# Kernel tuning notes

Measured on AMD Instinct MI355X. Metric: run time of the kernel, lower is better.

## Reference

```python
import jax, jax.numpy as jnp
import numpy as np
from jax import lax

B, C, H, W = 8, 128, 128, 128
KW = 9                      # conv window width (w == h == 9)
PW = (KW - 1) // 2


def _make_kernel(key):
    # torch kaiming_normal_(fan_out) on weight (C,1,KW,C): fan_out = C * KW * C
    std = float(np.sqrt(2.0 / (C * KW * C)))
    # stored directly in WIO layout: [KW, C_in, C_out]
    return (jax.random.normal(key, (KW, C, C), dtype=jnp.float32) * std)


def setup_inputs() -> dict:
    key = jax.random.key(0)
    kx, k1, k2, k3, k4 = jax.random.split(key, 5)
    x = jax.random.normal(kx, (B, C, H, W), dtype=jnp.float32)
    return {
        "x": x,
        "k_td": _make_kernel(k1),
        "k_dt": _make_kernel(k2),
        "k_lr": _make_kernel(k3),
        "k_rl": _make_kernel(k4),
    }


def _row_conv(y, K):
    # y: [B, W, C] -> 1D conv along W, full channel mixing, no bias
    return lax.conv_general_dilated(
        y, K, window_strides=(1,), padding=[(PW, PW)],
        dimension_numbers=("NWC", "WIO", "NWC"))


def _dir_scan(x, K, reverse):
    # x: [B, H, W, C]; sequential recurrence along axis 1:
    #   row[i] = row[i] + relu(conv(row[i-1]))   (row[i-1] already updated)
    if reverse:
        x = x[:, ::-1]
    def step(prev, cur):
        new = cur + jax.nn.relu(_row_conv(prev, K))
        return new, new
    first = x[:, 0]
    _, rest = lax.scan(step, first, jnp.moveaxis(x[:, 1:], 1, 0))
    out = jnp.concatenate([first[:, None], jnp.moveaxis(rest, 0, 1)], axis=1)
    if reverse:
        out = out[:, ::-1]
    return out


def reference(x, k_td, k_dt, k_lr, k_rl):
    y = jnp.transpose(x, (0, 2, 3, 1))        # [B, H, W, C]
    y = _dir_scan(y, k_td, reverse=False)      # top -> down
    y = _dir_scan(y, k_dt, reverse=True)       # down -> top
    yt = jnp.swapaxes(y, 1, 2)                 # [B, W, H, C]
    yt = _dir_scan(yt, k_lr, reverse=False)    # left -> right
    yt = _dir_scan(yt, k_rl, reverse=True)     # right -> left
    y = jnp.swapaxes(yt, 1, 2)
    return jnp.transpose(y, (0, 3, 1, 2))      # back to [B, C, H, W]
```

## Files before the change

kernel.cpp:

```cpp
#include <hip/hip_runtime.h>

#define B_   8
#define C_   128
#define HW_  128
#define KW_  9
#define BLKS 4
#define POSB 32
#define ROWS 40
#define STRD 136
#define BUFE (ROWS * STRD)
#define THREADS 512

typedef __bf16 bf16x8 __attribute__((ext_vector_type(8)));
typedef float  floatx4 __attribute__((ext_vector_type(4)));
typedef unsigned long long u64;

__device__ __forceinline__ unsigned short bf16rn(float f) {
  union { float f; unsigned u; } x; x.f = f;
  return (unsigned short)((x.u + 0x7fffu + ((x.u >> 16) & 1u)) >> 16);
}

__global__ __launch_bounds__(256) void nchw_to_nhwc(const float* __restrict__ x,
                                                    float* __restrict__ y) {
  __shared__ float tile[32][33];
  const int blk = blockIdx.x;
  const int b = blk >> 7, h = blk & 127;
  const int tx = threadIdx.x & 31, ty = threadIdx.x >> 5;
  for (int t = 0; t < 16; ++t) {
    const int c0 = (t >> 2) * 32, w0 = (t & 3) * 32;
#pragma unroll
    for (int i = 0; i < 4; ++i) {
      const int c = c0 + ty + i * 8;
      tile[ty + i * 8][tx] = x[(((long)b * C_ + c) * HW_ + h) * HW_ + w0 + tx];
    }
    __syncthreads();
#pragma unroll
    for (int i = 0; i < 4; ++i) {
      const int w = w0 + ty + i * 8;
      y[(((long)b * HW_ + h) * HW_ + w) * C_ + c0 + tx] = tile[tx][ty + i * 8];
    }
    __syncthreads();
  }
}

__global__ __launch_bounds__(256) void nhwc_to_nchw(const float* __restrict__ y,
                                                    float* __restrict__ out) {
  __shared__ float tile[32][33];
  const int blk = blockIdx.x;
  const int b = blk >> 7, h = blk & 127;
  const int tx = threadIdx.x & 31, ty = threadIdx.x >> 5;
  for (int t = 0; t < 16; ++t) {
    const int w0 = (t >> 2) * 32, c0 = (t & 3) * 32;
#pragma unroll
    for (int i = 0; i < 4; ++i) {
      const int w = w0 + ty + i * 8;
      tile[ty + i * 8][tx] = y[(((long)b * HW_ + h) * HW_ + w) * C_ + c0 + tx];
    }
    __syncthreads();
#pragma unroll
    for (int i = 0; i < 4; ++i) {
      const int c = c0 + ty + i * 8;
      out[(((long)b * C_ + c) * HW_ + h) * HW_ + w0 + tx] = tile[tx][ty + i * 8];
    }
    __syncthreads();
  }
}

__global__ __launch_bounds__(THREADS, 2) void scnn_scan_dir(
    const float* __restrict__ Kg, float* __restrict__ y,
    int* flags, u64* mb,
    const int posStride, const int sStride, const int s0, const int ds,
    const int dirIdx) {
  __shared__ unsigned short prow[2][BUFE];
  __shared__ float scratch[4 * 2 * 2 * 64 * 4];
  const int tid = threadIdx.x;
  const int bid = blockIdx.x;
  const int batch = bid & 7;
  const int blk = bid >> 3;
  const int p0 = blk * POSB;
  const int lane = tid & 63;
  const int wave = tid >> 6;
  const int kh = wave >> 2;
  const int co2 = wave & 3;
  const int l15 = lane & 15;
  const int quad = lane >> 4;
  const int ybase = batch * (HW_ * HW_ * C_);
  int* flagB = flags + (dirIdx * 8 + batch) * BLKS;

  for (int i = tid; i < 2 * BUFE / 4; i += THREADS)
    ((u64*)prow)[i] = 0ull;

  bf16x8 wfrag[2][KW_][2];
#pragma unroll
  for (int ct = 0; ct < 2; ++ct) {
    const int co0 = co2 * 16 + ct * 64;
#pragma unroll
    for (int kw = 0; kw < KW_; ++kw)
#pragma unroll
      for (int c2 = 0; c2 < 2; ++c2) {
        const int c4 = kh * 2 + c2;
        union { bf16x8 v; unsigned short u[8]; } t;
#pragma unroll
        for (int j = 0; j < 8; ++j)
          t.u[j] = bf16rn(Kg[(kw * 128 + c4 * 32 + quad * 8 + j) * 128 + co0 + l15]);
        wfrag[ct][kw][c2] = t.v;
      }
  }
  __syncthreads();

  for (int i = tid; i < ROWS * 32; i += THREADS) {
    const int row = i >> 5, cg = i & 31;
    const int pos = p0 - 4 + row;
    if (pos >= 0 && pos < HW_) {
      const floatx4 v =
          *(const floatx4*)&y[ybase + s0 * sStride + pos * posStride + cg * 4];
      union { u64 u; unsigned short s[4]; } t;
      t.s[0] = bf16rn(v[0]); t.s[1] = bf16rn(v[1]);
      t.s[2] = bf16rn(v[2]); t.s[3] = bf16rn(v[3]);
      *(u64*)&prow[0][row * STRD + cg * 4] = t.u;
    }
  }
  __syncthreads();

  int pb = 0;
#pragma unroll 1
  for (int s = 1; s < HW_; ++s) {
    const int srow = s0 + s * ds;
    const int rowb = ybase + srow * sStride;

    __syncthreads();
    if (tid == 0)
      __hip_atomic_store(&flagB[blk], s - 1, __ATOMIC_RELAXED,
                         __HIP_MEMORY_SCOPE_AGENT);
    if (s >= 2) {
      if (tid == 0 && blk > 0)
        while (__hip_atomic_load(&flagB[blk - 1], __ATOMIC_RELAXED,
                                 __HIP_MEMORY_SCOPE_AGENT) < s - 1)
          __builtin_amdgcn_s_sleep(1);
      if (tid == 1 && blk < BLKS - 1)
        while (__hip_atomic_load(&flagB[blk + 1], __ATOMIC_RELAXED,
                                 __HIP_MEMORY_SCOPE_AGENT) < s - 1)
          __builtin_amdgcn_s_sleep(1);
      __syncthreads();
      __atomic_signal_fence(__ATOMIC_SEQ_CST);
      const int par = (s - 1) & 1;
      if (tid < 256) {
        const int side = tid >> 7, p = (tid >> 5) & 3, cg = tid & 31;
        const bool doit = side ? (blk < BLKS - 1) : (blk > 0);
        if (doit) {
          const int srcB = side ? (blk + 1) : (blk - 1);
          const int srcSide = side ? 0 : 1;
          const int mbi =
              ((((batch * BLKS + srcB) * 2 + srcSide) * 2 + par) * 4 + p) * 32 + cg;
          const u64 v =
              __hip_atomic_load(&mb[mbi], __ATOMIC_RELAXED, __HIP_MEMORY_SCOPE_AGENT);
          const int row = side ? (36 + p) : p;
          *(u64*)&prow[pb][row * STRD + cg * 4] = v;
        }
      }
    }
    __syncthreads();

    floatx4 cur[2][2];
    if (kh == 0) {
#pragma unroll
      for (int ct = 0; ct < 2; ++ct)
#pragma unroll
        for (int n = 0; n < 2; ++n)
          cur[ct][n] = *(const floatx4*)&y[rowb + (p0 + n * 16 + l15) * posStride +
                                           co2 * 16 + ct * 64 + quad * 4];
    }

    floatx4 acc[2][2];
#pragma unroll
    for (int ct = 0; ct < 2; ++ct)
#pragma unroll
      for (int n = 0; n < 2; ++n)
        acc[ct][n] = floatx4{0.f, 0.f, 0.f, 0.f};

    const unsigned short* pbase = &prow[pb][l15 * STRD + quad * 8];
#pragma unroll
    for (int kw = 0; kw < KW_; ++kw)
#pragma unroll
      for (int c2 = 0; c2 < 2; ++c2) {
        const int c4 = kh * 2 + c2;
        const bf16x8 b0 = *(const bf16x8*)(pbase + kw * STRD + c4 * 32);
        const bf16x8 b1 = *(const bf16x8*)(pbase + (kw + 16) * STRD + c4 * 32);
        acc[0][0] = __builtin_amdgcn_mfma_f32_16x16x32_bf16(wfrag[0][kw][c2], b0,
                                                            acc[0][0], 0, 0, 0);
        acc[0][1] = __builtin_amdgcn_mfma_f32_16x16x32_bf16(wfrag[0][kw][c2], b1,
                                                            acc[0][1], 0, 0, 0);
        acc[1][0] = __builtin_amdgcn_mfma_f32_16x16x32_bf16(wfrag[1][kw][c2], b0,
                                                            acc[1][0], 0, 0, 0);
        acc[1][1] = __builtin_amdgcn_mfma_f32_16x16x32_bf16(wfrag[1][kw][c2], b1,
                                                            acc[1][1], 0, 0, 0);
      }

    if (kh == 1) {
#pragma unroll
      for (int ct = 0; ct < 2; ++ct)
#pragma unroll
        for (int n = 0; n < 2; ++n)
          *(floatx4*)&scratch[(((co2 * 2 + ct) * 2 + n) * 64 + lane) * 4] =
              acc[ct][n];
    }
    __syncthreads();

    if (kh == 0) {
#pragma unroll
      for (int ct = 0; ct < 2; ++ct)
#pragma unroll
        for (int n = 0; n < 2; ++n) {
          const floatx4 pz =
              *(const floatx4*)&scratch[(((co2 * 2 + ct) * 2 + n) * 64 + lane) * 4];
          acc[ct][n] += pz;
        }

      unsigned short* nxt = prow[pb ^ 1];
      const int par_w = s & 1;
#pragma unroll
      for (int ct = 0; ct < 2; ++ct) {
        const int co0 = co2 * 16 + ct * 64;
#pragma unroll
        for (int n = 0; n < 2; ++n) {
          const int pl = n * 16 + l15;
          const int co = co0 + quad * 4;
          const floatx4 a = acc[ct][n];
          const floatx4 c = cur[ct][n];
          floatx4 o;
          o[0] = c[0] + (a[0] > 0.f ? a[0] : 0.f);
          o[1] = c[1] + (a[1] > 0.f ? a[1] : 0.f);
          o[2] = c[2] + (a[2] > 0.f ? a[2] : 0.f);
          o[3] = c[3] + (a[3] > 0.f ? a[3] : 0.f);
          *(floatx4*)&y[rowb + (p0 + pl) * posStride + co] = o;
          union { u64 u; unsigned short s[4]; } t;
          t.s[0] = bf16rn(o[0]); t.s[1] = bf16rn(o[1]);
          t.s[2] = bf16rn(o[2]); t.s[3] = bf16rn(o[3]);
          *(u64*)&nxt[(pl + 4) * STRD + co] = t.u;
          if (n == 0 && l15 < 4 && blk > 0) {
            const int mbi =
                ((((batch * BLKS + blk) * 2 + 0) * 2 + par_w) * 4 + l15) * 32 +
                (co2 * 4 + ct * 16 + quad);
            __hip_atomic_store(&mb[mbi], t.u, __ATOMIC_RELAXED,
                               __HIP_MEMORY_SCOPE_AGENT);
          }
          if (n == 1 && l15 >= 12 && blk < BLKS - 1) {
            const int mbi =
                ((((batch * BLKS + blk) * 2 + 1) * 2 + par_w) * 4 + (l15 - 12)) * 32 +
                (co2 * 4 + ct * 16 + quad);
            __hip_atomic_store(&mb[mbi], t.u, __ATOMIC_RELAXED,
                               __HIP_MEMORY_SCOPE_AGENT);
          }
        }
      }
    }
    pb ^= 1;
  }
}

extern "C" void kernel_launch(void* const* d_in, const int* in_sizes, int n_in,
                              void* d_out, int out_size, void* d_ws, size_t ws_size,
                              hipStream_t stream) {
  const float* x = (const float*)d_in[0];
  const float* K[4] = {(const float*)d_in[1], (const float*)d_in[2],
                       (const float*)d_in[3], (const float*)d_in[4]};
  float* out = (float*)d_out;

  char* ws = (char*)d_ws;
  float* y = (float*)ws;
  int* flags = (int*)(ws + 67108864);
  u64* mb = (u64*)(ws + 67108864 + 1024);

  hipMemsetAsync(flags, 0, 1024, stream);
  nchw_to_nhwc<<<B_ * HW_, 256, 0, stream>>>(x, y);

  const int PS[4] = {C_, C_, HW_ * C_, HW_ * C_};
  const int SS[4] = {HW_ * C_, HW_ * C_, C_, C_};
  const int S0[4] = {0, HW_ - 1, 0, HW_ - 1};
  const int DS[4] = {1, -1, 1, -1};
  for (int d = 0; d < 4; ++d)
    scnn_scan_dir<<<B_ * BLKS, THREADS, 0, stream>>>(K[d], y, flags, mb, PS[d],
                                                     SS[d], S0[d], DS[d], d);

  nhwc_to_nchw<<<B_ * HW_, 256, 0, stream>>>(y, out);
}
```

Baseline: 2.222 ms.

## Split each scan row across eight blocks of sixteen positions per batch

Doubles the number of cooperating blocks per batch along the row (BLKS 4→8, 16 positions each), which halves the MFMA work per block per scan step and doubles total blocks from 32 to 64. The goal is to cut the critical-path compute per sequential step and use more CUs. In exchange, halo exchange and flag synchronization with neighbors are a larger share of each step, the halo rows are a larger fraction of the staged data, and more blocks must stay co-resident for the spin-wait protocol. Launch code and mailbox/flag sizing that are not shown must match the new block count.

```diff
diff --git a/kernel.cpp b/kernel.cpp
--- a/kernel.cpp
+++ b/kernel.cpp
@@ -4,9 +4,9 @@
 #define C_   128
 #define HW_  128
 #define KW_  9
-#define BLKS 4
-#define POSB 32
-#define ROWS 40
+#define BLKS 8
+#define POSB 16
+#define ROWS 24
 #define STRD 136
 #define BUFE (ROWS * STRD)
 #define THREADS 512
@@ -72,7 +72,7 @@
     const int posStride, const int sStride, const int s0, const int ds,
     const int dirIdx) {
   __shared__ unsigned short prow[2][BUFE];
-  __shared__ float scratch[4 * 2 * 2 * 64 * 4];
+  __shared__ float scratch[4 * 2 * 64 * 4];
   const int tid = threadIdx.x;
   const int bid = blockIdx.x;
   const int batch = bid & 7;
@@ -154,29 +154,24 @@
               ((((batch * BLKS + srcB) * 2 + srcSide) * 2 + par) * 4 + p) * 32 + cg;
           const u64 v =
               __hip_atomic_load(&mb[mbi], __ATOMIC_RELAXED, __HIP_MEMORY_SCOPE_AGENT);
-          const int row = side ? (36 + p) : p;
+          const int row = side ? (20 + p) : p;
           *(u64*)&prow[pb][row * STRD + cg * 4] = v;
         }
       }
     }
     __syncthreads();
 
-    floatx4 cur[2][2];
+    floatx4 cur[2];
     if (kh == 0) {
 #pragma unroll
       for (int ct = 0; ct < 2; ++ct)
-#pragma unroll
-        for (int n = 0; n < 2; ++n)
-          cur[ct][n] = *(const floatx4*)&y[rowb + (p0 + n * 16 + l15) * posStride +
-                                           co2 * 16 + ct * 64 + quad * 4];
-    }
-
-    floatx4 acc[2][2];
-#pragma unroll
-    for (int ct = 0; ct < 2; ++ct)
-#pragma unroll
-      for (int n = 0; n < 2; ++n)
-        acc[ct][n] = floatx4{0.f, 0.f, 0.f, 0.f};
+        cur[ct] = *(const floatx4*)&y[rowb + (p0 + l15) * posStride +
+                                      co2 * 16 + ct * 64 + quad * 4];
+    }
+
+    floatx4 acc[2];
+    acc[0] = floatx4{0.f, 0.f, 0.f, 0.f};
+    acc[1] = floatx4{0.f, 0.f, 0.f, 0.f};
 
     const unsigned short* pbase = &prow[pb][l15 * STRD + quad * 8];
 #pragma unroll
@@ -185,72 +180,59 @@
       for (int c2 = 0; c2 < 2; ++c2) {
         const int c4 = kh * 2 + c2;
         const bf16x8 b0 = *(const bf16x8*)(pbase + kw * STRD + c4 * 32);
-        const bf16x8 b1 = *(const bf16x8*)(pbase + (kw + 16) * STRD + c4 * 32);
-        acc[0][0] = __builtin_amdgcn_mfma_f32_16x16x32_bf16(wfrag[0][kw][c2], b0,
-                                                            acc[0][0], 0, 0, 0);
-        acc[0][1] = __builtin_amdgcn_mfma_f32_16x16x32_bf16(wfrag[0][kw][c2], b1,
-                                                            acc[0][1], 0, 0, 0);
-        acc[1][0] = __builtin_amdgcn_mfma_f32_16x16x32_bf16(wfrag[1][kw][c2], b0,
-                                                            acc[1][0], 0, 0, 0);
-        acc[1][1] = __builtin_amdgcn_mfma_f32_16x16x32_bf16(wfrag[1][kw][c2], b1,
-                                                            acc[1][1], 0, 0, 0);
+        acc[0] = __builtin_amdgcn_mfma_f32_16x16x32_bf16(wfrag[0][kw][c2], b0,
+                                                         acc[0], 0, 0, 0);
+        acc[1] = __builtin_amdgcn_mfma_f32_16x16x32_bf16(wfrag[1][kw][c2], b0,
+                                                         acc[1], 0, 0, 0);
       }
 
     if (kh == 1) {
 #pragma unroll
       for (int ct = 0; ct < 2; ++ct)
-#pragma unroll
-        for (int n = 0; n < 2; ++n)
-          *(floatx4*)&scratch[(((co2 * 2 + ct) * 2 + n) * 64 + lane) * 4] =
-              acc[ct][n];
+        *(floatx4*)&scratch[((co2 * 2 + ct) * 64 + lane) * 4] = acc[ct];
     }
     __syncthreads();
 
     if (kh == 0) {
 #pragma unroll
-      for (int ct = 0; ct < 2; ++ct)
-#pragma unroll
-        for (int n = 0; n < 2; ++n) {
-          const floatx4 pz =
-              *(const floatx4*)&scratch[(((co2 * 2 + ct) * 2 + n) * 64 + lane) * 4];
-          acc[ct][n] += pz;
-        }
+      for (int ct = 0; ct < 2; ++ct) {
+        const floatx4 pz =
+            *(const floatx4*)&scratch[((co2 * 2 + ct) * 64 + lane) * 4];
+        acc[ct] += pz;
+      }
 
       unsigned short* nxt = prow[pb ^ 1];
       const int par_w = s & 1;
 #pragma unroll
       for (int ct = 0; ct < 2; ++ct) {
         const int co0 = co2 * 16 + ct * 64;
-#pragma unroll
-        for (int n = 0; n < 2; ++n) {
-          const int pl = n * 16 + l15;
-          const int co = co0 + quad * 4;
-          const floatx4 a = acc[ct][n];
-          const floatx4 c = cur[ct][n];
-          floatx4 o;
-          o[0] = c[0] + (a[0] > 0.f ? a[0] : 0.f);
-          o[1] = c[1] + (a[1] > 0.f ? a[1] : 0.f);
-          o[2] = c[2] + (a[2] > 0.f ? a[2] : 0.f);
-          o[3] = c[3] + (a[3] > 0.f ? a[3] : 0.f);
-          *(floatx4*)&y[rowb + (p0 + pl) * posStride + co] = o;
-          union { u64 u; unsigned short s[4]; } t;
-          t.s[0] = bf16rn(o[0]); t.s[1] = bf16rn(o[1]);
-          t.s[2] = bf16rn(o[2]); t.s[3] = bf16rn(o[3]);
-          *(u64*)&nxt[(pl + 4) * STRD + co] = t.u;
-          if (n == 0 && l15 < 4 && blk > 0) {
-            const int mbi =
-                ((((batch * BLKS + blk) * 2 + 0) * 2 + par_w) * 4 + l15) * 32 +
-                (co2 * 4 + ct * 16 + quad);
-            __hip_atomic_store(&mb[mbi], t.u, __ATOMIC_RELAXED,
-                               __HIP_MEMORY_SCOPE_AGENT);
-          }
-          if (n == 1 && l15 >= 12 && blk < BLKS - 1) {
-            const int mbi =
-                ((((batch * BLKS + blk) * 2 + 1) * 2 + par_w) * 4 + (l15 - 12)) * 32 +
-                (co2 * 4 + ct * 16 + quad);
-            __hip_atomic_store(&mb[mbi], t.u, __ATOMIC_RELAXED,
-                               __HIP_MEMORY_SCOPE_AGENT);
-          }
+        const int pl = l15;
+        const int co = co0 + quad * 4;
+        const floatx4 a = acc[ct];
+        const floatx4 c = cur[ct];
+        floatx4 o;
+        o[0] = c[0] + (a[0] > 0.f ? a[0] : 0.f);
+        o[1] = c[1] + (a[1] > 0.f ? a[1] : 0.f);
+        o[2] = c[2] + (a[2] > 0.f ? a[2] : 0.f);
+        o[3] = c[3] + (a[3] > 0.f ? a[3] : 0.f);
+        *(floatx4*)&y[rowb + (p0 + pl) * posStride + co] = o;
+        union { u64 u; unsigned short s[4]; } t;
+        t.s[0] = bf16rn(o[0]); t.s[1] = bf16rn(o[1]);
+        t.s[2] = bf16rn(o[2]); t.s[3] = bf16rn(o[3]);
+        *(u64*)&nxt[(pl + 4) * STRD + co] = t.u;
+        if (l15 < 4 && blk > 0) {
+          const int mbi =
+              ((((batch * BLKS + blk) * 2 + 0) * 2 + par_w) * 4 + l15) * 32 +
+              (co2 * 4 + ct * 16 + quad);
+          __hip_atomic_store(&mb[mbi], t.u, __ATOMIC_RELAXED,
+                             __HIP_MEMORY_SCOPE_AGENT);
+        }
+        if (l15 >= 12 && blk < BLKS - 1) {
+          const int mbi =
+              ((((batch * BLKS + blk) * 2 + 1) * 2 + par_w) * 4 + (l15 - 12)) * 32 +
+              (co2 * 4 + ct * 16 + quad);
+          __hip_atomic_store(&mb[mbi], t.u, __ATOMIC_RELAXED,
+                             __HIP_MEMORY_SCOPE_AGENT);
         }
       }
     }
```

New measurement: 1.986 ms. 1.12x faster.
